# Performance work log

Hardware: AMD Instinct MI355X
Metric: run time of the kernel (lower is better)

The kernel has to match this reference:

```python
import jax, jax.numpy as jnp
import numpy as np

H = 128      # hidden_dim
D = 256      # 2*hidden_dim (transformer d_model)
NH = 4       # attention heads
EPS = 1e-5

def _bn(x, g, b):
    # BatchNorm1d, training mode: batch statistics over node axis (biased var)
    mu = x.mean(0)
    var = x.var(0)
    return (x - mu) / jnp.sqrt(var + EPS) * g + b

def _ln(x, g, b):
    mu = x.mean(-1, keepdims=True)
    var = x.var(-1, keepdims=True)
    return (x - mu) / jnp.sqrt(var + EPS) * g + b

def _sage(x_src, x_dst, src, dst, Wl, bl, Wr):
    # PyG SAGEConv(aggr='mean'): lin_l(mean_j x_src[src_j]) + lin_r(x_dst); lin_r has no bias
    n_dst = x_dst.shape[0]
    msg = x_src[src]  # [E, H] gather
    agg = jnp.zeros((n_dst, msg.shape[-1]), msg.dtype).at[dst].add(msg)
    cnt = jnp.zeros((n_dst,), msg.dtype).at[dst].add(1.0)
    agg = agg / jnp.maximum(cnt, 1.0)[:, None]
    return agg @ Wl + bl + x_dst @ Wr


def setup_inputs() -> dict:
    key = jax.random.key(0)
    T, NU, NT, FU, FT = 12, 10000, 2500, 64, 32
    E_tt, E_ut, E_tu = 50000, 100000, 100000
    L, TL, FFN = 3, 3, 256
    ks = iter(jax.random.split(key, 64))
    def nrm(shape, s=0.05):
        return jax.random.normal(next(ks), shape, jnp.float32) * s
    inp = {
        'x_user': nrm((T, NU, FU), 1.0),
        'x_tag': nrm((T, NT, FT), 1.0),
        'edge_tt': jax.random.randint(next(ks), (T, 2, E_tt), 0, NT),
        'edge_ut_src': jax.random.randint(next(ks), (T, E_ut), 0, NU),
        'edge_ut_dst': jax.random.randint(next(ks), (T, E_ut), 0, NT),
        'edge_tu_src': jax.random.randint(next(ks), (T, E_tu), 0, NT),
        'edge_tu_dst': jax.random.randint(next(ks), (T, E_tu), 0, NU),
        'bn_user_g': jnp.ones((FU,)), 'bn_user_b': jnp.zeros((FU,)),
        'bn_tag_g': jnp.ones((FT,)), 'bn_tag_b': jnp.zeros((FT,)),
        'proj_user_W': nrm((FU, H)), 'proj_user_b': jnp.zeros((H,)),
        'proj_tag_W': nrm((FT, H)), 'proj_tag_b': jnp.zeros((H,)),
        # conv params: axis0 = conv layer (3), axis1 = edge type (0:tt, 1:ut, 2:tu)
        'conv_Wl': nrm((L, 3, H, H)), 'conv_bl': jnp.zeros((L, 3, H)),
        'conv_Wr': nrm((L, 3, H, H)),
        'attn_Wq': nrm((TL, D, D)), 'attn_bq': jnp.zeros((TL, D)),
        'attn_Wk': nrm((TL, D, D)), 'attn_bk': jnp.zeros((TL, D)),
        'attn_Wv': nrm((TL, D, D)), 'attn_bv': jnp.zeros((TL, D)),
        'attn_Wo': nrm((TL, D, D)), 'attn_bo': jnp.zeros((TL, D)),
        'ln1_g': jnp.ones((TL, D)), 'ln1_b': jnp.zeros((TL, D)),
        'ffn_W1': nrm((TL, D, FFN)), 'ffn_b1': jnp.zeros((TL, FFN)),
        'ffn_W2': nrm((TL, FFN, D)), 'ffn_b2': jnp.zeros((TL, D)),
        'ln2_g': jnp.ones((TL, D)), 'ln2_b': jnp.zeros((TL, D)),
        'head_W': nrm((D, 4)), 'head_b': jnp.zeros((4,)),
    }
    return inp


def reference(x_user, x_tag, edge_tt, edge_ut_src, edge_ut_dst, edge_tu_src, edge_tu_dst,
              bn_user_g, bn_user_b, bn_tag_g, bn_tag_b,
              proj_user_W, proj_user_b, proj_tag_W, proj_tag_b,
              conv_Wl, conv_bl, conv_Wr,
              attn_Wq, attn_bq, attn_Wk, attn_bk, attn_Wv, attn_bv, attn_Wo, attn_bo,
              ln1_g, ln1_b, ffn_W1, ffn_b1, ffn_W2, ffn_b2, ln2_g, ln2_b,
              head_W, head_b):
    def month(xu, xt, e_tt, eus, eud, ets, etd):
        xu = _bn(xu, bn_user_g, bn_user_b) @ proj_user_W + proj_user_b
        xt = _bn(xt, bn_tag_g, bn_tag_b) @ proj_tag_W + proj_tag_b
        for l in range(conv_Wl.shape[0]):
            o_tt = _sage(xt, xt, e_tt[0], e_tt[1], conv_Wl[l, 0], conv_bl[l, 0], conv_Wr[l, 0])
            o_ut = _sage(xu, xt, eus, eud, conv_Wl[l, 1], conv_bl[l, 1], conv_Wr[l, 1])
            o_tu = _sage(xt, xu, ets, etd, conv_Wl[l, 2], conv_bl[l, 2], conv_Wr[l, 2])
            # HeteroConv aggr='mean': tag receives 2 relations, user receives 1
            xt = jax.nn.relu((o_tt + o_ut) * 0.5)
            xu = jax.nn.relu(o_tu)
        return jnp.concatenate([xu.mean(0), xt.mean(0)])  # [2H]

    emb = jax.vmap(month)(x_user, x_tag, edge_tt, edge_ut_src, edge_ut_dst,
                          edge_tu_src, edge_tu_dst)  # [12, 2H]
    x = emb[None]  # [1, 12, D]
    B, S, Dm = x.shape
    dh = Dm // NH
    scale = 1.0 / jnp.sqrt(jnp.float32(dh))
    for l in range(attn_Wq.shape[0]):
        q = (x @ attn_Wq[l] + attn_bq[l]).reshape(B, S, NH, dh)
        k = (x @ attn_Wk[l] + attn_bk[l]).reshape(B, S, NH, dh)
        v = (x @ attn_Wv[l] + attn_bv[l]).reshape(B, S, NH, dh)
        a = jax.nn.softmax(jnp.einsum('bqhd,bkhd->bhqk', q, k) * scale, axis=-1)
        o = jnp.einsum('bhqk,bkhd->bqhd', a, v).reshape(B, S, Dm) @ attn_Wo[l] + attn_bo[l]
        x = _ln(x + o, ln1_g[l], ln1_b[l])          # post-norm (norm_first=False)
        f = jax.nn.relu(x @ ffn_W1[l] + ffn_b1[l]) @ ffn_W2[l] + ffn_b2[l]
        x = _ln(x + f, ln2_g[l], ln2_b[l])
    # predictions: columns = [qpd, answer_rate, retention, growth]
    return x[:, -1, :] @ head_W + head_b  # [1, 4]
```

## Files before the change

kernel.cpp:

```cpp
#include <hip/hip_runtime.h>

constexpr int T = 12;
constexpr int NU = 10000;
constexpr int NT = 2500;
constexpr int FU = 64;
constexpr int FT = 32;
constexpr int H = 128;
constexpr int D = 256;
constexpr int E_TT = 50000;
constexpr int E_UT = 100000;
constexpr int E_TU = 100000;
constexpr float EPS = 1e-5f;

__device__ __forceinline__ void fma4(float4& a, const float4 x, const float4 w0,
                                     const float4 w1, const float4 w2, const float4 w3) {
  a.x += x.x * w0.x + x.y * w1.x + x.z * w2.x + x.w * w3.x;
  a.y += x.x * w0.y + x.y * w1.y + x.z * w2.y + x.w * w3.y;
  a.z += x.x * w0.z + x.y * w1.z + x.z * w2.z + x.w * w3.z;
  a.w += x.x * w0.w + x.y * w1.w + x.z * w2.w + x.w * w3.w;
}
__device__ __forceinline__ void add4(float4& a, const float4 v) {
  a.x += v.x; a.y += v.y; a.z += v.z; a.w += v.w;
}

__global__ __launch_bounds__(256) void bnsum_kernel(
    const float* __restrict__ x, int N, int F, float* __restrict__ sum,
    float* __restrict__ sq, int bpm) {
  int m = blockIdx.x / bpm, bc = blockIdx.x % bpm;
  int g = 256 / F;
  int c = threadIdx.x % F, rg = threadIdx.x / F;
  int rows = (N + bpm - 1) / bpm;
  int lo = bc * rows, hi = min(N, lo + rows);
  float s = 0.f, q = 0.f;
  for (int r = lo + rg; r < hi; r += g) {
    float v = x[((long)m * N + r) * F + c];
    s += v; q += v * v;
  }
  __shared__ float ssm[256], qsm[256];
  ssm[threadIdx.x] = s; qsm[threadIdx.x] = q;
  __syncthreads();
  if (rg == 0) {
    for (int i = 1; i < g; ++i) { s += ssm[i * F + c]; q += qsm[i * F + c]; }
    atomicAdd(&sum[m * F + c], s);
    atomicAdd(&sq[m * F + c], q);
  }
}

template <int F>
__global__ __launch_bounds__(256) void proj_kernel(
    const float* __restrict__ x, const float* __restrict__ sum, const float* __restrict__ sq,
    const float* __restrict__ g, const float* __restrict__ b,
    const float* __restrict__ W, const float* __restrict__ pb,
    float* __restrict__ out, int N, int chunks) {
  constexpr int RPB = 32;
  constexpr int KG = F / 4;
  int m = blockIdx.x / chunks, chunk = blockIdx.x % chunks;
  int row0 = chunk * RPB;
  int nr = min(RPB, N - row0);
  int tid = threadIdx.x;
  int cg = tid & 31, rg = tid >> 5;
  int c4 = cg * 4, r0 = rg * 4;
  __shared__ __align__(16) float A[RPB][F];
  __shared__ __align__(16) float scv[F], shv[F];
  if (tid < F) {
    float mu = sum[m * F + tid] * (1.f / N);
    float var = sq[m * F + tid] * (1.f / N) - mu * mu;
    float inv = rsqrtf(var + EPS);
    float s = g[tid] * inv;
    scv[tid] = s; shv[tid] = b[tid] - mu * s;
  }
  __syncthreads();
  const float* xb = x + ((long)m * N + row0) * F;
  for (int i = tid; i < nr * KG; i += 256) {
    int r = i / KG, k4 = (i % KG) * 4;
    float4 xv = *(const float4*)&xb[r * F + k4];
    float4 s4 = *(const float4*)&scv[k4];
    float4 h4 = *(const float4*)&shv[k4];
    float4 a;
    a.x = xv.x * s4.x + h4.x; a.y = xv.y * s4.y + h4.y;
    a.z = xv.z * s4.z + h4.z; a.w = xv.w * s4.w + h4.w;
    *(float4*)&A[r][k4] = a;
  }
  __syncthreads();
  float4 acc[4] = {{0,0,0,0},{0,0,0,0},{0,0,0,0},{0,0,0,0}};
  for (int k = 0; k < F; k += 4) {
    float4 w0 = *(const float4*)&W[(k + 0) * H + c4];
    float4 w1 = *(const float4*)&W[(k + 1) * H + c4];
    float4 w2 = *(const float4*)&W[(k + 2) * H + c4];
    float4 w3 = *(const float4*)&W[(k + 3) * H + c4];
#pragma unroll
    for (int r = 0; r < 4; ++r)
      fma4(acc[r], *(const float4*)&A[r0 + r][k], w0, w1, w2, w3);
  }
  float4 bias = *(const float4*)&pb[c4];
  float* ob = out + ((long)m * N + row0) * H;
#pragma unroll
  for (int r = 0; r < 4; ++r)
    if (r0 + r < nr) {
      float4 o4;
      o4.x = acc[r].x + bias.x; o4.y = acc[r].y + bias.y;
      o4.z = acc[r].z + bias.z; o4.w = acc[r].w + bias.w;
      *(float4*)&ob[(r0 + r) * H + c4] = o4;
    }
}

__global__ __launch_bounds__(256) void count_kernel(
    const int* __restrict__ dst, long mstride, int E, int* __restrict__ cnt, int N) {
  long idx = (long)blockIdx.x * 256 + threadIdx.x;
  if (idx >= (long)T * E) return;
  int m = (int)(idx / E), e = (int)(idx % E);
  int d = dst[m * mstride + e];
  atomicAdd(&cnt[m * N + d], 1);
}

__global__ __launch_bounds__(1024) void scan_kernel(
    int* __restrict__ iw, long cnt_tt, long off_tt, long cur_tt,
    long cnt_ut, long off_ut, long cur_ut,
    long cnt_tu, long off_tu, long cur_tu) {
  int b = blockIdx.x;
  int type = b / 12, m = b % 12;
  const int* cnt; int* off; int* cur; int N;
  if (type == 0) {
    cnt = iw + cnt_tt + (long)m * NT; off = iw + off_tt + (long)m * (NT + 1);
    cur = iw + cur_tt + (long)m * NT; N = NT;
  } else if (type == 1) {
    cnt = iw + cnt_ut + (long)m * NT; off = iw + off_ut + (long)m * (NT + 1);
    cur = iw + cur_ut + (long)m * NT; N = NT;
  } else {
    cnt = iw + cnt_tu + (long)m * NU; off = iw + off_tu + (long)m * (NU + 1);
    cur = iw + cur_tu + (long)m * NU; N = NU;
  }
  __shared__ int s[1024];
  int tid = threadIdx.x;
  int running = 0;
  for (int base = 0; base < N; base += 1024) {
    int i = base + tid;
    int v = (i < N) ? cnt[i] : 0;
    s[tid] = v;
    __syncthreads();
    for (int o = 1; o < 1024; o <<= 1) {
      int t = (tid >= o) ? s[tid - o] : 0;
      __syncthreads();
      s[tid] += t;
      __syncthreads();
    }
    if (i < N) { int e = running + s[tid] - v; off[i] = e; cur[i] = e; }
    int tot = s[1023];
    __syncthreads();
    running += tot;
  }
  if (tid == 0) off[N] = running;
}

__global__ __launch_bounds__(256) void fill_kernel(
    const int* __restrict__ src, long sstride, const int* __restrict__ dst, long dstride,
    int E, int* __restrict__ cur, int N, int* __restrict__ srcs) {
  long idx = (long)blockIdx.x * 256 + threadIdx.x;
  if (idx >= (long)T * E) return;
  int m = (int)(idx / E), e = (int)(idx % E);
  int d = dst[m * dstride + e];
  int sv = src[m * sstride + e];
  int pos = atomicAdd(&cur[m * N + d], 1);
  srcs[(long)m * E + pos] = sv;
}

__global__ __launch_bounds__(256) void combine_wr_kernel(
    const float* __restrict__ Wr, float* __restrict__ wrc) {
  int i = blockIdx.x * 256 + threadIdx.x;
  int l = i / (H * H), j = i % (H * H);
  wrc[i] = Wr[(long)(l * 3 + 0) * H * H + j] + Wr[(long)(l * 3 + 1) * H * H + j];
}

__global__ __launch_bounds__(256) void agg_kernel(
    const int* __restrict__ off, const int* __restrict__ srcs,
    const float* __restrict__ xsrc, float* __restrict__ agg,
    int Ndst, int Nsrc, int E, int chunks) {
  int m = blockIdx.x / chunks, chunk = blockIdx.x % chunks;
  int slot = threadIdx.x >> 5;
  int c4 = (threadIdx.x & 31) * 4;
  int row = chunk * 8 + slot;
  if (row >= Ndst) return;
  const int* o = off + (long)m * (Ndst + 1);
  int o0 = o[row], o1 = o[row + 1];
  const int* sp = srcs + (long)m * E;
  const float* xb = xsrc + (long)m * Nsrc * H;
  float4 a0 = {0,0,0,0}, a1 = {0,0,0,0}, a2 = {0,0,0,0}, a3 = {0,0,0,0};
  int j = o0;
  for (; j + 3 < o1; j += 4) {
    int s0 = sp[j], s1 = sp[j + 1], s2 = sp[j + 2], s3 = sp[j + 3];
    add4(a0, *(const float4*)&xb[(long)s0 * H + c4]);
    add4(a1, *(const float4*)&xb[(long)s1 * H + c4]);
    add4(a2, *(const float4*)&xb[(long)s2 * H + c4]);
    add4(a3, *(const float4*)&xb[(long)s3 * H + c4]);
  }
  for (; j < o1; ++j) add4(a0, *(const float4*)&xb[(long)sp[j] * H + c4]);
  add4(a0, a1); add4(a2, a3); add4(a0, a2);
  float inv = 1.f / (float)max(o1 - o0, 1);
  a0.x *= inv; a0.y *= inv; a0.z *= inv; a0.w *= inv;
  *(float4*)&agg[((long)m * Ndst + row) * H + c4] = a0;
}

__global__ __launch_bounds__(256) void update_tag_kernel(
    float* __restrict__ xt, const float* __restrict__ aggtt, const float* __restrict__ aggut,
    const float* __restrict__ Wl, const float* __restrict__ bl, const float* __restrict__ wrc,
    int layer, int chunks) {
  int m = blockIdx.x / chunks, chunk = blockIdx.x % chunks;
  int row0 = chunk * 32;
  int nr = min(32, NT - row0);
  int tid = threadIdx.x;
  int cg = tid & 31, rg = tid >> 5;
  int c4 = cg * 4, r0 = rg * 4;
  __shared__ __align__(16) float sm0[32][H], sm1[32][H], sm2[32][H];
  const float* p0 = aggtt + ((long)m * NT + row0) * H;
  const float* p1 = xt + ((long)m * NT + row0) * H;
  const float* p2 = aggut + ((long)m * NT + row0) * H;
  for (int i = tid; i < nr * 32; i += 256) {
    int r = i >> 5, k4 = (i & 31) * 4;
    *(float4*)&sm0[r][k4] = *(const float4*)&p0[r * H + k4];
    *(float4*)&sm1[r][k4] = *(const float4*)&p1[r * H + k4];
    *(float4*)&sm2[r][k4] = *(const float4*)&p2[r * H + k4];
  }
  __syncthreads();
  const float* wl0 = Wl + (long)(layer * 3 + 0) * H * H;
  const float* wl1 = Wl + (long)(layer * 3 + 1) * H * H;
  const float* wc = wrc + (long)layer * H * H;
  float4 acc[4] = {{0,0,0,0},{0,0,0,0},{0,0,0,0},{0,0,0,0}};
  for (int k = 0; k < H; k += 4) {
    float4 u0 = *(const float4*)&wl0[(k + 0) * H + c4];
    float4 u1 = *(const float4*)&wl0[(k + 1) * H + c4];
    float4 u2 = *(const float4*)&wl0[(k + 2) * H + c4];
    float4 u3 = *(const float4*)&wl0[(k + 3) * H + c4];
    float4 v0 = *(const float4*)&wc[(k + 0) * H + c4];
    float4 v1 = *(const float4*)&wc[(k + 1) * H + c4];
    float4 v2 = *(const float4*)&wc[(k + 2) * H + c4];
    float4 v3 = *(const float4*)&wc[(k + 3) * H + c4];
    float4 t0 = *(const float4*)&wl1[(k + 0) * H + c4];
    float4 t1 = *(const float4*)&wl1[(k + 1) * H + c4];
    float4 t2 = *(const float4*)&wl1[(k + 2) * H + c4];
    float4 t3 = *(const float4*)&wl1[(k + 3) * H + c4];
#pragma unroll
    for (int r = 0; r < 4; ++r) {
      fma4(acc[r], *(const float4*)&sm0[r0 + r][k], u0, u1, u2, u3);
      fma4(acc[r], *(const float4*)&sm1[r0 + r][k], v0, v1, v2, v3);
      fma4(acc[r], *(const float4*)&sm2[r0 + r][k], t0, t1, t2, t3);
    }
  }
  float4 b0 = *(const float4*)&bl[(long)(layer * 3 + 0) * H + c4];
  float4 b1 = *(const float4*)&bl[(long)(layer * 3 + 1) * H + c4];
  float* ob = xt + ((long)m * NT + row0) * H;
#pragma unroll
  for (int r = 0; r < 4; ++r)
    if (r0 + r < nr) {
      float4 o4;
      o4.x = fmaxf(0.f, 0.5f * (acc[r].x + b0.x + b1.x));
      o4.y = fmaxf(0.f, 0.5f * (acc[r].y + b0.y + b1.y));
      o4.z = fmaxf(0.f, 0.5f * (acc[r].z + b0.z + b1.z));
      o4.w = fmaxf(0.f, 0.5f * (acc[r].w + b0.w + b1.w));
      *(float4*)&ob[(r0 + r) * H + c4] = o4;
    }
}

__global__ __launch_bounds__(256) void update_user_kernel(
    float* __restrict__ xu, const float* __restrict__ aggtu,
    const float* __restrict__ Wl, const float* __restrict__ bl, const float* __restrict__ Wr,
    int layer, int chunks) {
  int m = blockIdx.x / chunks, chunk = blockIdx.x % chunks;
  int row0 = chunk * 32;
  int nr = min(32, NU - row0);
  int tid = threadIdx.x;
  int cg = tid & 31, rg = tid >> 5;
  int c4 = cg * 4, r0 = rg * 4;
  __shared__ __align__(16) float sm0[32][H], sm1[32][H];
  const float* p0 = aggtu + ((long)m * NU + row0) * H;
  const float* p1 = xu + ((long)m * NU + row0) * H;
  for (int i = tid; i < nr * 32; i += 256) {
    int r = i >> 5, k4 = (i & 31) * 4;
    *(float4*)&sm0[r][k4] = *(const float4*)&p0[r * H + k4];
    *(float4*)&sm1[r][k4] = *(const float4*)&p1[r * H + k4];
  }
  __syncthreads();
  const float* wl = Wl + (long)(layer * 3 + 2) * H * H;
  const float* wr = Wr + (long)(layer * 3 + 2) * H * H;
  float4 acc[4] = {{0,0,0,0},{0,0,0,0},{0,0,0,0},{0,0,0,0}};
  for (int k = 0; k < H; k += 4) {
    float4 u0 = *(const float4*)&wl[(k + 0) * H + c4];
    float4 u1 = *(const float4*)&wl[(k + 1) * H + c4];
    float4 u2 = *(const float4*)&wl[(k + 2) * H + c4];
    float4 u3 = *(const float4*)&wl[(k + 3) * H + c4];
    float4 v0 = *(const float4*)&wr[(k + 0) * H + c4];
    float4 v1 = *(const float4*)&wr[(k + 1) * H + c4];
    float4 v2 = *(const float4*)&wr[(k + 2) * H + c4];
    float4 v3 = *(const float4*)&wr[(k + 3) * H + c4];
#pragma unroll
    for (int r = 0; r < 4; ++r) {
      fma4(acc[r], *(const float4*)&sm0[r0 + r][k], u0, u1, u2, u3);
      fma4(acc[r], *(const float4*)&sm1[r0 + r][k], v0, v1, v2, v3);
    }
  }
  float4 bias = *(const float4*)&bl[(long)(layer * 3 + 2) * H + c4];
  float* ob = xu + ((long)m * NU + row0) * H;
#pragma unroll
  for (int r = 0; r < 4; ++r)
    if (r0 + r < nr) {
      float4 o4;
      o4.x = fmaxf(0.f, acc[r].x + bias.x);
      o4.y = fmaxf(0.f, acc[r].y + bias.y);
      o4.z = fmaxf(0.f, acc[r].z + bias.z);
      o4.w = fmaxf(0.f, acc[r].w + bias.w);
      *(float4*)&ob[(r0 + r) * H + c4] = o4;
    }
}

__global__ __launch_bounds__(256) void pool_kernel(
    const float* __restrict__ x, int N, float* __restrict__ emb, int base, int bpm) {
  int m = blockIdx.x / bpm, bc = blockIdx.x % bpm;
  int cg = threadIdx.x & 31, rg = threadIdx.x >> 5;
  int c4 = cg * 4;
  int rows = (N + bpm - 1) / bpm;
  int lo = bc * rows, hi = min(N, lo + rows);
  float4 acc = {0,0,0,0};
  for (int r = lo + rg; r < hi; r += 8)
    add4(acc, *(const float4*)&x[((long)m * N + r) * H + c4]);
  __shared__ __align__(16) float4 sm[8][32];
  sm[rg][cg] = acc;
  __syncthreads();
  if (rg == 0) {
    float4 s = sm[0][cg];
#pragma unroll
    for (int i = 1; i < 8; ++i) add4(s, sm[i][cg]);
    float inv = 1.f / (float)N;
    atomicAdd(&emb[m * D + base + c4 + 0], s.x * inv);
    atomicAdd(&emb[m * D + base + c4 + 1], s.y * inv);
    atomicAdd(&emb[m * D + base + c4 + 2], s.z * inv);
    atomicAdd(&emb[m * D + base + c4 + 3], s.w * inv);
  }
}

__device__ __forceinline__ void mm_slice(const float (&Xs)[12][256], const float* __restrict__ W,
                                         int ks, int tid, float* __restrict__ pOut) {
  int cg = tid & 63, rg = tid >> 6;
  int c4 = cg * 4;
  int s0 = rg * 3;
  float4 a0 = {0, 0, 0, 0}, a1 = {0, 0, 0, 0}, a2 = {0, 0, 0, 0};
  for (int k = ks * 64; k < ks * 64 + 64; k += 4) {
    float4 w0 = *(const float4*)&W[(k + 0) * 256 + c4];
    float4 w1 = *(const float4*)&W[(k + 1) * 256 + c4];
    float4 w2 = *(const float4*)&W[(k + 2) * 256 + c4];
    float4 w3 = *(const float4*)&W[(k + 3) * 256 + c4];
    fma4(a0, *(const float4*)&Xs[s0 + 0][k], w0, w1, w2, w3);
    fma4(a1, *(const float4*)&Xs[s0 + 1][k], w0, w1, w2, w3);
    fma4(a2, *(const float4*)&Xs[s0 + 2][k], w0, w1, w2, w3);
  }
  *(float4*)&pOut[(s0 + 0) * 256 + c4] = a0;
  *(float4*)&pOut[(s0 + 1) * 256 + c4] = a1;
  *(float4*)&pOut[(s0 + 2) * 256 + c4] = a2;
}

__device__ __forceinline__ void ln_rows(float (&Xs)[12][256], const float* __restrict__ g,
                                        const float* __restrict__ b, float (&rs)[4],
                                        float (&rq)[4], int tid) {
  for (int s = 0; s < 12; ++s) {
    float v = Xs[s][tid];
    float sm_ = v, sq_ = v * v;
    for (int o = 32; o > 0; o >>= 1) {
      sm_ += __shfl_down(sm_, o);
      sq_ += __shfl_down(sq_, o);
    }
    if ((tid & 63) == 0) { rs[tid >> 6] = sm_; rq[tid >> 6] = sq_; }
    __syncthreads();
    float mu = (rs[0] + rs[1] + rs[2] + rs[3]) * (1.f / 256);
    float var = (rq[0] + rq[1] + rq[2] + rq[3]) * (1.f / 256) - mu * mu;
    Xs[s][tid] = (v - mu) * rsqrtf(var + EPS) * g[tid] + b[tid];
    __syncthreads();
  }
}

__global__ __launch_bounds__(256) void trans_qkv(
    const float* __restrict__ xb, const float* __restrict__ pF2, const float* __restrict__ x1v,
    const float* __restrict__ b2, const float* __restrict__ ln2g, const float* __restrict__ ln2b,
    float* __restrict__ xb_out,
    const float* __restrict__ Wq, const float* __restrict__ Wk, const float* __restrict__ Wv,
    float* __restrict__ pQKV, int fuse) {
  __shared__ float Xs[12][256];
  __shared__ float rs[4], rq[4];
  int tid = threadIdx.x;
  int mat = blockIdx.x >> 2, ks = blockIdx.x & 3;
  if (fuse) {
    for (int s = 0; s < 12; ++s) {
      int i = s * 256 + tid;
      Xs[s][tid] = pF2[i] + pF2[3072 + i] + pF2[6144 + i] + pF2[9216 + i] + b2[tid] + x1v[i];
    }
    __syncthreads();
    ln_rows(Xs, ln2g, ln2b, rs, rq, tid);
    if (blockIdx.x == 0)
      for (int s = 0; s < 12; ++s) xb_out[s * 256 + tid] = Xs[s][tid];
  } else {
    for (int s = 0; s < 12; ++s) Xs[s][tid] = xb[s * 256 + tid];
    __syncthreads();
  }
  const float* W = (mat == 0) ? Wq : (mat == 1) ? Wk : Wv;
  mm_slice(Xs, W, ks, tid, pQKV + (mat * 4 + ks) * 3072);
}

__global__ __launch_bounds__(256) void trans_attn(
    const float* __restrict__ pQKV, const float* __restrict__ bq,
    const float* __restrict__ bk, const float* __restrict__ bv, float* __restrict__ O) {
  __shared__ float Qs[12][256], Ksh[12][256], Vs[12][256];
  __shared__ float Sc[4][12][12];
  int tid = threadIdx.x;
  for (int s = 0; s < 12; ++s) {
    int i = s * 256 + tid;
    const float* p = pQKV;
    Qs[s][tid] = p[i] + p[3072 + i] + p[6144 + i] + p[9216 + i] + bq[tid];
    p = pQKV + 12288;
    Ksh[s][tid] = p[i] + p[3072 + i] + p[6144 + i] + p[9216 + i] + bk[tid];
    p = pQKV + 24576;
    Vs[s][tid] = p[i] + p[3072 + i] + p[6144 + i] + p[9216 + i] + bv[tid];
  }
  __syncthreads();
  for (int idx = tid; idx < 576; idx += 256) {
    int h = idx / 144, rem = idx % 144, qi = rem / 12, ti = rem % 12;
    float acc = 0.f;
    for (int d = 0; d < 64; d += 4) {
      float4 qv = *(const float4*)&Qs[qi][h * 64 + d];
      float4 kv = *(const float4*)&Ksh[ti][h * 64 + d];
      acc += qv.x * kv.x + qv.y * kv.y + qv.z * kv.z + qv.w * kv.w;
    }
    Sc[h][qi][ti] = acc * 0.125f;
  }
  __syncthreads();
  if (tid < 48) {
    int h = tid / 12, qi = tid % 12;
    float mx = -1e30f;
    for (int t2 = 0; t2 < 12; ++t2) mx = fmaxf(mx, Sc[h][qi][t2]);
    float e[12], sum = 0.f;
    for (int t2 = 0; t2 < 12; ++t2) { e[t2] = __expf(Sc[h][qi][t2] - mx); sum += e[t2]; }
    float inv = 1.f / sum;
    for (int t2 = 0; t2 < 12; ++t2) Sc[h][qi][t2] = e[t2] * inv;
  }
  __syncthreads();
  int h = tid >> 6;
#pragma unroll
  for (int s = 0; s < 12; ++s) {
    float acc = 0.f;
#pragma unroll
    for (int t2 = 0; t2 < 12; ++t2) acc += Sc[h][s][t2] * Vs[t2][tid];
    O[s * 256 + tid] = acc;
  }
}

__global__ __launch_bounds__(256) void trans_mm(
    const float* __restrict__ In, const float* __restrict__ W, float* __restrict__ pOut) {
  __shared__ float Xs[12][256];
  int tid = threadIdx.x, ks = blockIdx.x;
  for (int s = 0; s < 12; ++s) Xs[s][tid] = In[s * 256 + tid];
  __syncthreads();
  mm_slice(Xs, W, ks, tid, pOut + ks * 3072);
}

__global__ __launch_bounds__(256) void trans_ffn1(
    const float* __restrict__ pP, const float* __restrict__ bo, const float* __restrict__ xb,
    const float* __restrict__ ln1g, const float* __restrict__ ln1b, float* __restrict__ x1_out,
    const float* __restrict__ W1, float* __restrict__ pF1) {
  __shared__ float Xs[12][256];
  __shared__ float rs[4], rq[4];
  int tid = threadIdx.x, ks = blockIdx.x;
  for (int s = 0; s < 12; ++s) {
    int i = s * 256 + tid;
    Xs[s][tid] = pP[i] + pP[3072 + i] + pP[6144 + i] + pP[9216 + i] + bo[tid] + xb[i];
  }
  __syncthreads();
  ln_rows(Xs, ln1g, ln1b, rs, rq, tid);
  if (ks == 0)
    for (int s = 0; s < 12; ++s) x1_out[s * 256 + tid] = Xs[s][tid];
  mm_slice(Xs, W1, ks, tid, pF1 + ks * 3072);
}

__global__ __launch_bounds__(256) void trans_ffn2(
    const float* __restrict__ pF1, const float* __restrict__ b1,
    const float* __restrict__ W2, float* __restrict__ pF2) {
  __shared__ float Xs[12][256];
  int tid = threadIdx.x, ks = blockIdx.x;
  for (int s = 0; s < 12; ++s) {
    int i = s * 256 + tid;
    Xs[s][tid] = fmaxf(0.f, pF1[i] + pF1[3072 + i] + pF1[6144 + i] + pF1[9216 + i] + b1[tid]);
  }
  __syncthreads();
  mm_slice(Xs, W2, ks, tid, pF2 + ks * 3072);
}

__global__ __launch_bounds__(256) void trans_head(
    const float* __restrict__ pF2, const float* __restrict__ b2, const float* __restrict__ x1v,
    const float* __restrict__ ln2g, const float* __restrict__ ln2b,
    const float* __restrict__ hW, const float* __restrict__ hb, float* __restrict__ out) {
  __shared__ float h[256];
  __shared__ float rs[4], rq[4];
  int tid = threadIdx.x;
  int i = 11 * 256 + tid;
  float v = pF2[i] + pF2[3072 + i] + pF2[6144 + i] + pF2[9216 + i] + b2[tid] + x1v[i];
  float sm_ = v, sq_ = v * v;
  for (int o = 32; o > 0; o >>= 1) { sm_ += __shfl_down(sm_, o); sq_ += __shfl_down(sq_, o); }
  if ((tid & 63) == 0) { rs[tid >> 6] = sm_; rq[tid >> 6] = sq_; }
  __syncthreads();
  float mu = (rs[0] + rs[1] + rs[2] + rs[3]) * (1.f / 256);
  float var = (rq[0] + rq[1] + rq[2] + rq[3]) * (1.f / 256) - mu * mu;
  h[tid] = (v - mu) * rsqrtf(var + EPS) * ln2g[tid] + ln2b[tid];
  __syncthreads();
  if (tid < 4) {
    float acc = hb[tid];
    for (int k = 0; k < 256; ++k) acc += h[k] * hW[k * 4 + tid];
    out[tid] = acc;
  }
}

extern "C" void kernel_launch(void* const* d_in, const int* in_sizes, int n_in,
                              void* d_out, int out_size, void* d_ws, size_t ws_size,
                              hipStream_t stream) {
  (void)in_sizes; (void)n_in; (void)out_size; (void)ws_size;
  const float* x_user = (const float*)d_in[0];
  const float* x_tag  = (const float*)d_in[1];
  const int* edge_tt  = (const int*)d_in[2];
  const int* e_us     = (const int*)d_in[3];
  const int* e_ud     = (const int*)d_in[4];
  const int* e_ts     = (const int*)d_in[5];
  const int* e_td     = (const int*)d_in[6];
  const float* bn_ug  = (const float*)d_in[7];
  const float* bn_ub  = (const float*)d_in[8];
  const float* bn_tg  = (const float*)d_in[9];
  const float* bn_tb  = (const float*)d_in[10];
  const float* pu_W   = (const float*)d_in[11];
  const float* pu_b   = (const float*)d_in[12];
  const float* pt_W   = (const float*)d_in[13];
  const float* pt_b   = (const float*)d_in[14];
  const float* cWl    = (const float*)d_in[15];
  const float* cbl    = (const float*)d_in[16];
  const float* cWr    = (const float*)d_in[17];
  const float* aWq    = (const float*)d_in[18];
  const float* abq    = (const float*)d_in[19];
  const float* aWk    = (const float*)d_in[20];
  const float* abk    = (const float*)d_in[21];
  const float* aWv    = (const float*)d_in[22];
  const float* abv    = (const float*)d_in[23];
  const float* aWo    = (const float*)d_in[24];
  const float* abo    = (const float*)d_in[25];
  const float* l1g    = (const float*)d_in[26];
  const float* l1b    = (const float*)d_in[27];
  const float* fW1    = (const float*)d_in[28];
  const float* fb1    = (const float*)d_in[29];
  const float* fW2    = (const float*)d_in[30];
  const float* fb2    = (const float*)d_in[31];
  const float* l2g    = (const float*)d_in[32];
  const float* l2b    = (const float*)d_in[33];
  const float* hW     = (const float*)d_in[34];
  const float* hb     = (const float*)d_in[35];

  float* ws = (float*)d_ws;
  int* iw = (int*)d_ws;
  size_t o = 0;
  auto alloc = [&](size_t n) { size_t r = o; o += n; return r; };
  size_t sum_u = alloc(T * FU), sq_u = alloc(T * FU);
  size_t sum_t = alloc(T * FT), sq_t = alloc(T * FT);
  size_t cnt_tt = alloc((size_t)T * NT), cnt_ut = alloc((size_t)T * NT), cnt_tu = alloc((size_t)T * NU);
  size_t emb = alloc(T * D);
  size_t zeroElems = o;
  size_t off_tt = alloc((size_t)T * (NT + 1)), off_ut = alloc((size_t)T * (NT + 1)), off_tu = alloc((size_t)T * (NU + 1));
  size_t cur_tt = alloc((size_t)T * NT), cur_ut = alloc((size_t)T * NT), cur_tu = alloc((size_t)T * NU);
  size_t srcs_tt = alloc((size_t)T * E_TT), srcs_ut = alloc((size_t)T * E_UT), srcs_tu = alloc((size_t)T * E_TU);
  size_t xu = alloc((size_t)T * NU * H), xt = alloc((size_t)T * NT * H);
  size_t agg_tt = alloc((size_t)T * NT * H), agg_ut = alloc((size_t)T * NT * H), agg_tu = alloc((size_t)T * NU * H);

  size_t wrc  = cnt_tt;
  size_t pQKV = cnt_tt + 49152;
  size_t pP   = cnt_tt + 86016;
  size_t pF1  = cnt_tt + 98304;
  size_t pF2  = cnt_tt + 110592;
  size_t Ob   = cnt_tt + 122880;
  size_t x1b  = cnt_tt + 125952;

  (void)hipMemsetAsync(d_ws, 0, zeroElems * sizeof(float), stream);

  bnsum_kernel<<<dim3(T * 8), 256, 0, stream>>>(x_user, NU, FU, ws + sum_u, ws + sq_u, 8);
  bnsum_kernel<<<dim3(T * 4), 256, 0, stream>>>(x_tag, NT, FT, ws + sum_t, ws + sq_t, 4);
  int pch_u = (NU + 31) / 32, pch_t = (NT + 31) / 32;
  proj_kernel<FU><<<dim3(T * pch_u), 256, 0, stream>>>(
      x_user, ws + sum_u, ws + sq_u, bn_ug, bn_ub, pu_W, pu_b, ws + xu, NU, pch_u);
  proj_kernel<FT><<<dim3(T * pch_t), 256, 0, stream>>>(
      x_tag, ws + sum_t, ws + sq_t, bn_tg, bn_tb, pt_W, pt_b, ws + xt, NT, pch_t);
  count_kernel<<<dim3((T * E_TT + 255) / 256), 256, 0, stream>>>(edge_tt + E_TT, 2L * E_TT, E_TT, iw + cnt_tt, NT);
  count_kernel<<<dim3((T * E_UT + 255) / 256), 256, 0, stream>>>(e_ud, E_UT, E_UT, iw + cnt_ut, NT);
  count_kernel<<<dim3((T * E_TU + 255) / 256), 256, 0, stream>>>(e_td, E_TU, E_TU, iw + cnt_tu, NU);
  scan_kernel<<<dim3(36), 1024, 0, stream>>>(iw, (long)cnt_tt, (long)off_tt, (long)cur_tt,
                                             (long)cnt_ut, (long)off_ut, (long)cur_ut,
                                             (long)cnt_tu, (long)off_tu, (long)cur_tu);
  combine_wr_kernel<<<dim3(192), 256, 0, stream>>>(cWr, ws + wrc);
  fill_kernel<<<dim3((T * E_TT + 255) / 256), 256, 0, stream>>>(edge_tt, 2L * E_TT, edge_tt + E_TT, 2L * E_TT, E_TT, iw + cur_tt, NT, iw + srcs_tt);
  fill_kernel<<<dim3((T * E_UT + 255) / 256), 256, 0, stream>>>(e_us, E_UT, e_ud, E_UT, E_UT, iw + cur_ut, NT, iw + srcs_ut);
  fill_kernel<<<dim3((T * E_TU + 255) / 256), 256, 0, stream>>>(e_ts, E_TU, e_td, E_TU, E_TU, iw + cur_tu, NU, iw + srcs_tu);
  int ach_t = (NT + 7) / 8, ach_u = (NU + 7) / 8;
  int uch_t = (NT + 31) / 32, uch_u = (NU + 31) / 32;
  for (int l = 0; l < 3; ++l) {
    agg_kernel<<<dim3(T * ach_t), 256, 0, stream>>>(iw + off_tt, iw + srcs_tt, ws + xt, ws + agg_tt, NT, NT, E_TT, ach_t);
    agg_kernel<<<dim3(T * ach_t), 256, 0, stream>>>(iw + off_ut, iw + srcs_ut, ws + xu, ws + agg_ut, NT, NU, E_UT, ach_t);
    agg_kernel<<<dim3(T * ach_u), 256, 0, stream>>>(iw + off_tu, iw + srcs_tu, ws + xt, ws + agg_tu, NU, NT, E_TU, ach_u);
    update_tag_kernel<<<dim3(T * uch_t), 256, 0, stream>>>(ws + xt, ws + agg_tt, ws + agg_ut, cWl, cbl, ws + wrc, l, uch_t);
    update_user_kernel<<<dim3(T * uch_u), 256, 0, stream>>>(ws + xu, ws + agg_tu, cWl, cbl, cWr, l, uch_u);
  }
  pool_kernel<<<dim3(T * 16), 256, 0, stream>>>(ws + xu, NU, ws + emb, 0, 16);
  pool_kernel<<<dim3(T * 8), 256, 0, stream>>>(ws + xt, NT, ws + emb, H, 8);
  long DD = (long)D * D;
  for (int l = 0; l < 3; ++l) {
    int fuse = (l > 0);
    int lp = fuse ? (l - 1) : 0;
    trans_qkv<<<dim3(12), 256, 0, stream>>>(
        ws + emb, ws + pF2, ws + x1b, fb2 + lp * D, l2g + lp * D, l2b + lp * D, ws + emb,
        aWq + l * DD, aWk + l * DD, aWv + l * DD, ws + pQKV, fuse);
    trans_attn<<<dim3(1), 256, 0, stream>>>(ws + pQKV, abq + l * D, abk + l * D, abv + l * D, ws + Ob);
    trans_mm<<<dim3(4), 256, 0, stream>>>(ws + Ob, aWo + l * DD, ws + pP);
    trans_ffn1<<<dim3(4), 256, 0, stream>>>(ws + pP, abo + l * D, ws + emb, l1g + l * D, l1b + l * D,
                                            ws + x1b, fW1 + l * DD, ws + pF1);
    trans_ffn2<<<dim3(4), 256, 0, stream>>>(ws + pF1, fb1 + l * D, fW2 + l * DD, ws + pF2);
  }
  trans_head<<<dim3(1), 256, 0, stream>>>(ws + pF2, fb2 + 2 * D, ws + x1b, l2g + 2 * D, l2b + 2 * D,
                                          hW, hb, (float*)d_out);
}
```

Measured before the change: 2.453 ms.

## Drop LDS staging in SAGE update kernels and tile 16 rows per thread

Both node-update kernels no longer stage activation tiles in shared memory. Each thread now reads its 16 rows directly from global memory and computes two output columns. Every 64-lane wave shares the same row addresses, so those loads become uniform broadcasts, and each weight load is reused across 16 rows instead of 4. This removes the LDS copy and barrier at the cost of more accumulator registers and less memory-level parallelism per block. The in-place update stays safe because each wave reads all of its rows before writing them.

```diff
diff --git a/kernel.cpp b/kernel.cpp
--- a/kernel.cpp
+++ b/kernel.cpp
@@ -200,114 +200,136 @@
   *(float4*)&agg[((long)m * Ndst + row) * H + c4] = a0;
 }
 
+__global__ __launch_bounds__(256) void update_user_kernel(
+    float* __restrict__ xu, const float* __restrict__ aggtu,
+    const float* __restrict__ Wl, const float* __restrict__ bl, const float* __restrict__ Wr,
+    int layer, int chunks) {
+  constexpr int RPB = 64, RPT = 16;
+  int m = blockIdx.x / chunks, chunk = blockIdx.x % chunks;
+  int row0 = chunk * RPB;
+  int tid = threadIdx.x;
+  int c2 = (tid & 63) * 2;
+  int r0 = (tid >> 6) * RPT;
+  const float* wl = Wl + (long)(layer * 3 + 2) * H * H;
+  const float* wr = Wr + (long)(layer * 3 + 2) * H * H;
+  const float* ab = aggtu + (long)m * NU * H;
+  const float* xb = xu + (long)m * NU * H;
+  int rows[RPT];
+#pragma unroll
+  for (int r = 0; r < RPT; ++r) rows[r] = min(row0 + r0 + r, NU - 1);
+  float2 acc[RPT];
+#pragma unroll
+  for (int r = 0; r < RPT; ++r) acc[r] = {0.f, 0.f};
+  for (int k = 0; k < H; k += 4) {
+    {
+      float2 w0 = *(const float2*)&wl[(k + 0) * H + c2];
+      float2 w1 = *(const float2*)&wl[(k + 1) * H + c2];
+      float2 w2 = *(const float2*)&wl[(k + 2) * H + c2];
+      float2 w3 = *(const float2*)&wl[(k + 3) * H + c2];
+#pragma unroll
+      for (int r = 0; r < RPT; ++r) {
+        float4 xv = *(const float4*)&ab[(long)rows[r] * H + k];
+        acc[r].x += xv.x * w0.x + xv.y * w1.x + xv.z * w2.x + xv.w * w3.x;
+        acc[r].y += xv.x * w0.y + xv.y * w1.y + xv.z * w2.y + xv.w * w3.y;
+      }
+    }
+    {
+      float2 w0 = *(const float2*)&wr[(k + 0) * H + c2];
+      float2 w1 = *(const float2*)&wr[(k + 1) * H + c2];
+      float2 w2 = *(const float2*)&wr[(k + 2) * H + c2];
+      float2 w3 = *(const float2*)&wr[(k + 3) * H + c2];
+#pragma unroll
+      for (int r = 0; r < RPT; ++r) {
+        float4 xv = *(const float4*)&xb[(long)rows[r] * H + k];
+        acc[r].x += xv.x * w0.x + xv.y * w1.x + xv.z * w2.x + xv.w * w3.x;
+        acc[r].y += xv.x * w0.y + xv.y * w1.y + xv.z * w2.y + xv.w * w3.y;
+      }
+    }
+  }
+  float2 bias = *(const float2*)&bl[(long)(layer * 3 + 2) * H + c2];
+  int nr = min(RPB, NU - row0);
+  float* ob = xu + ((long)m * NU + row0) * H;
+#pragma unroll
+  for (int r = 0; r < RPT; ++r)
+    if (r0 + r < nr) {
+      float2 o2;
+      o2.x = fmaxf(0.f, acc[r].x + bias.x);
+      o2.y = fmaxf(0.f, acc[r].y + bias.y);
+      *(float2*)&ob[(r0 + r) * H + c2] = o2;
+    }
+}
+
 __global__ __launch_bounds__(256) void update_tag_kernel(
     float* __restrict__ xt, const float* __restrict__ aggtt, const float* __restrict__ aggut,
     const float* __restrict__ Wl, const float* __restrict__ bl, const float* __restrict__ wrc,
     int layer, int chunks) {
+  constexpr int RPB = 64, RPT = 16;
   int m = blockIdx.x / chunks, chunk = blockIdx.x % chunks;
-  int row0 = chunk * 32;
-  int nr = min(32, NT - row0);
+  int row0 = chunk * RPB;
   int tid = threadIdx.x;
-  int cg = tid & 31, rg = tid >> 5;
-  int c4 = cg * 4, r0 = rg * 4;
-  __shared__ __align__(16) float sm0[32][H], sm1[32][H], sm2[32][H];
-  const float* p0 = aggtt + ((long)m * NT + row0) * H;
-  const float* p1 = xt + ((long)m * NT + row0) * H;
-  const float* p2 = aggut + ((long)m * NT + row0) * H;
-  for (int i = tid; i < nr * 32; i += 256) {
-    int r = i >> 5, k4 = (i & 31) * 4;
-    *(float4*)&sm0[r][k4] = *(const float4*)&p0[r * H + k4];
-    *(float4*)&sm1[r][k4] = *(const float4*)&p1[r * H + k4];
-    *(float4*)&sm2[r][k4] = *(const float4*)&p2[r * H + k4];
-  }
-  __syncthreads();
+  int c2 = (tid & 63) * 2;
+  int r0 = (tid >> 6) * RPT;
   const float* wl0 = Wl + (long)(layer * 3 + 0) * H * H;
   const float* wl1 = Wl + (long)(layer * 3 + 1) * H * H;
   const float* wc = wrc + (long)layer * H * H;
-  float4 acc[4] = {{0,0,0,0},{0,0,0,0},{0,0,0,0},{0,0,0,0}};
+  const float* a0b = aggtt + (long)m * NT * H;
+  const float* xb = xt + (long)m * NT * H;
+  const float* a1b = aggut + (long)m * NT * H;
+  int rows[RPT];
+#pragma unroll
+  for (int r = 0; r < RPT; ++r) rows[r] = min(row0 + r0 + r, NT - 1);
+  float2 acc[RPT];
+#pragma unroll
+  for (int r = 0; r < RPT; ++r) acc[r] = {0.f, 0.f};
   for (int k = 0; k < H; k += 4) {
-    float4 u0 = *(const float4*)&wl0[(k + 0) * H + c4];
-    float4 u1 = *(const float4*)&wl0[(k + 1) * H + c4];
-    float4 u2 = *(const float4*)&wl0[(k + 2) * H + c4];
-    float4 u3 = *(const float4*)&wl0[(k + 3) * H + c4];
-    float4 v0 = *(const float4*)&wc[(k + 0) * H + c4];
-    float4 v1 = *(const float4*)&wc[(k + 1) * H + c4];
-    float4 v2 = *(const float4*)&wc[(k + 2) * H + c4];
-    float4 v3 = *(const float4*)&wc[(k + 3) * H + c4];
-    float4 t0 = *(const float4*)&wl1[(k + 0) * H + c4];
-    float4 t1 = *(const float4*)&wl1[(k + 1) * H + c4];
-    float4 t2 = *(const float4*)&wl1[(k + 2) * H + c4];
-    float4 t3 = *(const float4*)&wl1[(k + 3) * H + c4];
-#pragma unroll
-    for (int r = 0; r < 4; ++r) {
-      fma4(acc[r], *(const float4*)&sm0[r0 + r][k], u0, u1, u2, u3);
-      fma4(acc[r], *(const float4*)&sm1[r0 + r][k], v0, v1, v2, v3);
-      fma4(acc[r], *(const float4*)&sm2[r0 + r][k], t0, t1, t2, t3);
-    }
-  }
-  float4 b0 = *(const float4*)&bl[(long)(layer * 3 + 0) * H + c4];
-  float4 b1 = *(const float4*)&bl[(long)(layer * 3 + 1) * H + c4];
+    {
+      float2 w0 = *(const float2*)&wl0[(k + 0) * H + c2];
+      float2 w1 = *(const float2*)&wl0[(k + 1) * H + c2];
+      float2 w2 = *(const float2*)&wl0[(k + 2) * H + c2];
+      float2 w3 = *(const float2*)&wl0[(k + 3) * H + c2];
+#pragma unroll
+      for (int r = 0; r < RPT; ++r) {
+        float4 xv = *(const float4*)&a0b[(long)rows[r] * H + k];
+        acc[r].x += xv.x * w0.x + xv.y * w1.x + xv.z * w2.x + xv.w * w3.x;
+        acc[r].y += xv.x * w0.y + xv.y * w1.y + xv.z * w2.y + xv.w * w3.y;
+      }
+    }
+    {
+      float2 w0 = *(const float2*)&wc[(k + 0) * H + c2];
+      float2 w1 = *(const float2*)&wc[(k + 1) * H + c2];
+      float2 w2 = *(const float2*)&wc[(k + 2) * H + c2];
+      float2 w3 = *(const float2*)&wc[(k + 3) * H + c2];
+#pragma unroll
+      for (int r = 0; r < RPT; ++r) {
+        float4 xv = *(const float4*)&xb[(long)rows[r] * H + k];
+        acc[r].x += xv.x * w0.x + xv.y * w1.x + xv.z * w2.x + xv.w * w3.x;
+        acc[r].y += xv.x * w0.y + xv.y * w1.y + xv.z * w2.y + xv.w * w3.y;
+      }
+    }
+    {
+      float2 w0 = *(const float2*)&wl1[(k + 0) * H + c2];
+      float2 w1 = *(const float2*)&wl1[(k + 1) * H + c2];
+      float2 w2 = *(const float2*)&wl1[(k + 2) * H + c2];
+      float2 w3 = *(const float2*)&wl1[(k + 3) * H + c2];
+#pragma unroll
+      for (int r = 0; r < RPT; ++r) {
+        float4 xv = *(const float4*)&a1b[(long)rows[r] * H + k];
+        acc[r].x += xv.x * w0.x + xv.y * w1.x + xv.z * w2.x + xv.w * w3.x;
+        acc[r].y += xv.x * w0.y + xv.y * w1.y + xv.z * w2.y + xv.w * w3.y;
+      }
+    }
+  }
+  float2 b0 = *(const float2*)&bl[(long)(layer * 3 + 0) * H + c2];
+  float2 b1 = *(const float2*)&bl[(long)(layer * 3 + 1) * H + c2];
+  int nr = min(RPB, NT - row0);
   float* ob = xt + ((long)m * NT + row0) * H;
 #pragma unroll
-  for (int r = 0; r < 4; ++r)
+  for (int r = 0; r < RPT; ++r)
     if (r0 + r < nr) {
-      float4 o4;
-      o4.x = fmaxf(0.f, 0.5f * (acc[r].x + b0.x + b1.x));
-      o4.y = fmaxf(0.f, 0.5f * (acc[r].y + b0.y + b1.y));
-      o4.z = fmaxf(0.f, 0.5f * (acc[r].z + b0.z + b1.z));
-      o4.w = fmaxf(0.f, 0.5f * (acc[r].w + b0.w + b1.w));
-      *(float4*)&ob[(r0 + r) * H + c4] = o4;
-    }
-}
-
-__global__ __launch_bounds__(256) void update_user_kernel(
-    float* __restrict__ xu, const float* __restrict__ aggtu,
-    const float* __restrict__ Wl, const float* __restrict__ bl, const float* __restrict__ Wr,
-    int layer, int chunks) {
-  int m = blockIdx.x / chunks, chunk = blockIdx.x % chunks;
-  int row0 = chunk * 32;
-  int nr = min(32, NU - row0);
-  int tid = threadIdx.x;
-  int cg = tid & 31, rg = tid >> 5;
-  int c4 = cg * 4, r0 = rg * 4;
-  __shared__ __align__(16) float sm0[32][H], sm1[32][H];
-  const float* p0 = aggtu + ((long)m * NU + row0) * H;
-  const float* p1 = xu + ((long)m * NU + row0) * H;
-  for (int i = tid; i < nr * 32; i += 256) {
-    int r = i >> 5, k4 = (i & 31) * 4;
-    *(float4*)&sm0[r][k4] = *(const float4*)&p0[r * H + k4];
-    *(float4*)&sm1[r][k4] = *(const float4*)&p1[r * H + k4];
-  }
-  __syncthreads();
-  const float* wl = Wl + (long)(layer * 3 + 2) * H * H;
-  const float* wr = Wr + (long)(layer * 3 + 2) * H * H;
-  float4 acc[4] = {{0,0,0,0},{0,0,0,0},{0,0,0,0},{0,0,0,0}};
-  for (int k = 0; k < H; k += 4) {
-    float4 u0 = *(const float4*)&wl[(k + 0) * H + c4];
-    float4 u1 = *(const float4*)&wl[(k + 1) * H + c4];
-    float4 u2 = *(const float4*)&wl[(k + 2) * H + c4];
-    float4 u3 = *(const float4*)&wl[(k + 3) * H + c4];
-    float4 v0 = *(const float4*)&wr[(k + 0) * H + c4];
-    float4 v1 = *(const float4*)&wr[(k + 1) * H + c4];
-    float4 v2 = *(const float4*)&wr[(k + 2) * H + c4];
-    float4 v3 = *(const float4*)&wr[(k + 3) * H + c4];
-#pragma unroll
-    for (int r = 0; r < 4; ++r) {
-      fma4(acc[r], *(const float4*)&sm0[r0 + r][k], u0, u1, u2, u3);
-      fma4(acc[r], *(const float4*)&sm1[r0 + r][k], v0, v1, v2, v3);
-    }
-  }
-  float4 bias = *(const float4*)&bl[(long)(layer * 3 + 2) * H + c4];
-  float* ob = xu + ((long)m * NU + row0) * H;
-#pragma unroll
-  for (int r = 0; r < 4; ++r)
-    if (r0 + r < nr) {
-      float4 o4;
-      o4.x = fmaxf(0.f, acc[r].x + bias.x);
-      o4.y = fmaxf(0.f, acc[r].y + bias.y);
-      o4.z = fmaxf(0.f, acc[r].z + bias.z);
-      o4.w = fmaxf(0.f, acc[r].w + bias.w);
-      *(float4*)&ob[(r0 + r) * H + c4] = o4;
+      float2 o2;
+      o2.x = fmaxf(0.f, 0.5f * (acc[r].x + b0.x + b1.x));
+      o2.y = fmaxf(0.f, 0.5f * (acc[r].y + b0.y + b1.y));
+      *(float2*)&ob[(r0 + r) * H + c2] = o2;
     }
 }
 
@@ -597,7 +619,7 @@
   fill_kernel<<<dim3((T * E_UT + 255) / 256), 256, 0, stream>>>(e_us, E_UT, e_ud, E_UT, E_UT, iw + cur_ut, NT, iw + srcs_ut);
   fill_kernel<<<dim3((T * E_TU + 255) / 256), 256, 0, stream>>>(e_ts, E_TU, e_td, E_TU, E_TU, iw + cur_tu, NU, iw + srcs_tu);
   int ach_t = (NT + 7) / 8, ach_u = (NU + 7) / 8;
-  int uch_t = (NT + 31) / 32, uch_u = (NU + 31) / 32;
+  int uch_t = (NT + 63) / 64, uch_u = (NU + 63) / 64;
   for (int l = 0; l < 3; ++l) {
     agg_kernel<<<dim3(T * ach_t), 256, 0, stream>>>(iw + off_tt, iw + srcs_tt, ws + xt, ws + agg_tt, NT, NT, E_TT, ach_t);
     agg_kernel<<<dim3(T * ach_t), 256, 0, stream>>>(iw + off_ut, iw + srcs_ut, ws + xu, ws + agg_ut, NT, NU, E_UT, ach_t);
```

Result: slower. 2.843 ms (+15.9%).
